# Kernel tuning notes

Measured on AMD Instinct MI355X. Metric: run time of the kernel, lower is better.

## Reference

```python
import jax, jax.numpy as jnp
import numpy as np

N_VERTS = 100000
N_JOINTS = 24
N_BETAS = 10
N_POSEDIRS = 207  # (24-1)*9
# Standard SMPL kinematic tree parents
PARENTS = np.array([-1, 0, 0, 0, 1, 2, 3, 4, 5, 6, 7, 8, 9, 9, 9, 12, 13, 14, 16, 17, 18, 19, 20, 21])


def setup_inputs() -> dict:
    key = jax.random.key(0)
    ks = jax.random.split(key, 9)
    f = jnp.float32
    return {
        "betas": jax.random.normal(ks[0], (N_BETAS,), f),
        "pose": jax.random.normal(ks[1], (N_JOINTS, 3), f) * 0.2,
        "scale": jnp.ones((1,), f),
        "trans": jax.random.normal(ks[2], (3,), f),
        "v_template": jax.random.normal(ks[3], (N_VERTS, 3), f),
        "shapedirs": jax.random.normal(ks[4], (N_VERTS, 3, N_BETAS), f) * 0.01,
        "posedirs": jax.random.normal(ks[5], (N_VERTS, 3, N_POSEDIRS), f) * 0.01,
        "J_regressor": jax.random.uniform(ks[6], (N_JOINTS, N_VERTS), f) / N_VERTS,
        "weights": jax.nn.softmax(jax.random.normal(ks[7], (N_VERTS, N_JOINTS), f), axis=-1),
    }


def rodrigues(r):
    """Axis-angle [J,3] -> rotation matrices [J,3,3] (matches torch impl; eps kept tiny+deterministic)."""
    theta = jnp.linalg.norm(r + 1e-8, axis=-1, keepdims=True)  # [J,1]
    r_hat = r / theta
    z = jnp.zeros_like(r_hat[:, 0])
    K = jnp.stack([z, -r_hat[:, 2], r_hat[:, 1],
                   r_hat[:, 2], z, -r_hat[:, 0],
                   -r_hat[:, 1], r_hat[:, 0], z], axis=1).reshape(-1, 3, 3)
    c = jnp.cos(theta)[..., None]  # [J,1,1]
    s = jnp.sin(theta)[..., None]
    outer = r_hat[:, :, None] * r_hat[:, None, :]  # [J,3,3]
    I = jnp.eye(3, dtype=r.dtype)
    return c * I + (1.0 - c) * outer + s * K


def reference(betas, pose, scale, trans, v_template, shapedirs, posedirs, J_regressor, weights):
    dt = v_template.dtype
    # blend shapes
    v_shaped = jnp.einsum('vks,s->vk', shapedirs, betas) + v_template  # [V,3]
    J = J_regressor @ v_shaped  # [24,3]
    R = rodrigues(pose)  # [24,3,3]
    I3 = jnp.eye(3, dtype=dt)
    lrotmin = (R[1:] - I3).reshape(-1)  # [207]
    v_posed = v_shaped + jnp.einsum('vkp,p->vk', posedirs, lrotmin)  # [V,3]
    # forward kinematics over 24-joint chain
    bottom = jnp.array([[0.0, 0.0, 0.0, 1.0]], dtype=dt)
    def make_A(Ri, t):
        return jnp.concatenate([jnp.concatenate([Ri, t[:, None]], axis=1), bottom], axis=0)  # [4,4]
    As = [make_A(R[0], J[0])]
    for i in range(1, N_JOINTS):
        p = int(PARENTS[i])
        As.append(As[p] @ make_A(R[i], J[i] - J[p]))
    G = jnp.stack(As)  # [24,4,4]
    # remove rest-pose joint locations
    Jh = jnp.concatenate([J, jnp.zeros((N_JOINTS, 1), dt)], axis=1)  # [24,4]
    corr = jnp.einsum('jab,jb->ja', G, Jh)  # [24,4]
    rel = G - jnp.concatenate([jnp.zeros((N_JOINTS, 4, 3), dt), corr[:, :, None]], axis=2)
    # linear blend skinning
    T = jnp.einsum('vj,jab->vab', weights, rel)  # [V,4,4]
    vh = jnp.concatenate([v_posed, jnp.ones((v_posed.shape[0], 1), dt)], axis=1)  # [V,4]
    v = jnp.einsum('vab,vb->va', T, vh)[:, :3]  # [V,3]
    return v * scale.reshape(()) + trans[None, :]
```

## Files before the change

kernel.cpp:

```cpp
#include <hip/hip_runtime.h>

#define NV 100000
#define NJ 24
#define NP 207
#define NPART 25
#define NQUADS (NV / 4)
#define GRIDF 512
#define NWV (GRIDF * 4)

__device__ __forceinline__ float dpp_red32(float x) {
  x += __int_as_float(__builtin_amdgcn_update_dpp(0, __float_as_int(x), 0x111, 0xf, 0xf, true));
  x += __int_as_float(__builtin_amdgcn_update_dpp(0, __float_as_int(x), 0x112, 0xf, 0xf, true));
  x += __int_as_float(__builtin_amdgcn_update_dpp(0, __float_as_int(x), 0x114, 0xf, 0xf, true));
  x += __int_as_float(__builtin_amdgcn_update_dpp(0, __float_as_int(x), 0x118, 0xf, 0xf, true));
  x += __int_as_float(__builtin_amdgcn_update_dpp(0, __float_as_int(x), 0x142, 0xf, 0xf, true));
  return x;
}

__global__ __launch_bounds__(256) void k_shape(
    const float* __restrict__ betas, const float* __restrict__ v_template,
    const float* __restrict__ shapedirs, float* __restrict__ v_shaped) {
  __shared__ float sb[10];
  if (threadIdx.x < 10) sb[threadIdx.x] = betas[threadIdx.x];
  __syncthreads();
  int t = blockIdx.x * 256 + threadIdx.x;
  if (t >= 3 * NV / 2) return;
  const float4* sd4 = (const float4*)(shapedirs + (size_t)t * 20);
  float4 f0 = sd4[0], f1 = sd4[1], f2 = sd4[2], f3 = sd4[3], f4v = sd4[4];
  float2 vt = ((const float2*)v_template)[t];
  float a = vt.x
          + f0.x * sb[0] + f0.y * sb[1] + f0.z * sb[2] + f0.w * sb[3]
          + f1.x * sb[4] + f1.y * sb[5] + f1.z * sb[6] + f1.w * sb[7]
          + f2.x * sb[8] + f2.y * sb[9];
  float b = vt.y
          + f2.z * sb[0] + f2.w * sb[1]
          + f3.x * sb[2] + f3.y * sb[3] + f3.z * sb[4] + f3.w * sb[5]
          + f4v.x * sb[6] + f4v.y * sb[7] + f4v.z * sb[8] + f4v.w * sb[9];
  ((float2*)v_shaped)[t] = make_float2(a, b);
}

__global__ __launch_bounds__(256) void k_jreg(
    const float* __restrict__ Jreg, const float* __restrict__ v_shaped,
    float* __restrict__ jpT) {
  int j = blockIdx.x, part = blockIdx.y, tid = threadIdx.x;
  const int SL = NV / NPART;
  int v0 = part * SL;
  const float4* w4 = (const float4*)(Jreg + (size_t)j * NV + v0);
  const float4* s4 = (const float4*)(v_shaped + (size_t)3 * v0);
  float s0 = 0.f, s1 = 0.f, s2 = 0.f;
  for (int i4 = tid; i4 < SL / 4; i4 += 256) {
    float4 w = w4[i4];
    float4 A = s4[3 * i4 + 0];
    float4 B = s4[3 * i4 + 1];
    float4 C = s4[3 * i4 + 2];
    s0 += w.x * A.x + w.y * A.w + w.z * B.z + w.w * C.y;
    s1 += w.x * A.y + w.y * B.x + w.z * B.w + w.w * C.z;
    s2 += w.x * A.z + w.y * B.y + w.z * C.x + w.w * C.w;
  }
  __shared__ float red[256][3];
  red[tid][0] = s0; red[tid][1] = s1; red[tid][2] = s2;
  __syncthreads();
  for (int off = 128; off > 0; off >>= 1) {
    if (tid < off) {
      red[tid][0] += red[tid + off][0];
      red[tid][1] += red[tid + off][1];
      red[tid][2] += red[tid + off][2];
    }
    __syncthreads();
  }
  if (tid < 3) jpT[(j * 3 + tid) * 32 + part] = red[0][tid];
}

__device__ __forceinline__ void stage_quad(float4* dst, const float4* src, int lane) {
  #pragma unroll
  for (int r = 0; r < 10; ++r) {
    int i4 = r * 64 + lane;
    int i4c = (i4 < 621) ? i4 : 620;
    __builtin_amdgcn_global_load_lds(
        (const __attribute__((address_space(1))) void*)(src + i4c),
        (__attribute__((address_space(3))) void*)(dst + r * 64),
        16, 0, 0);
  }
}

__global__ __launch_bounds__(256, 2) void k_fused(
    const float* __restrict__ posedirs, const float* __restrict__ wgt,
    const float* __restrict__ pose, const float* __restrict__ jpT,
    const float* __restrict__ scale, const float* __restrict__ trans,
    float* __restrict__ vbuf) {
  __shared__ float4 buf[4][2][640];
  int tid = threadIdx.x, b = blockIdx.x;
  int wid = tid >> 6, lane = tid & 63, half = lane >> 5, lj = lane & 31;
  int W = b * 4 + wid;
  const float4* pd4 = (const float4*)posedirs;

  int q0 = W;
  float pvl0 = (lj < 3) ? vbuf[(size_t)3 * (q0 * 4 + half) + lj] : 0.f;
  float wj0  = (lj < NJ) ? wgt[(size_t)(q0 * 4 + half) * NJ + lj] : 0.f;
  float pvl1 = (lj < 3) ? vbuf[(size_t)3 * (q0 * 4 + 2 + half) + lj] : 0.f;
  float wj1  = (lj < NJ) ? wgt[(size_t)(q0 * 4 + 2 + half) * NJ + lj] : 0.f;
  __builtin_amdgcn_sched_barrier(0);
  stage_quad(&buf[wid][0][0], pd4 + (size_t)q0 * 621, lane);

  float* fkJ  = (float*)&buf[0][1][0];
  float* fkR  = fkJ + 72;
  float* fkG  = fkJ + 288;
  float* lrs  = fkJ + 576;
  float* relS = fkJ + 784;
  if (tid < NJ * 3) {
    const float* src = jpT + tid * 32;
    float a = 0.f;
    #pragma unroll
    for (int i = 0; i < NPART; ++i) a += src[i];
    fkJ[tid] = a;
  }
  if (tid < NJ) {
    float rx = pose[tid * 3 + 0], ry = pose[tid * 3 + 1], rz = pose[tid * 3 + 2];
    float tx = rx + 1e-8f, ty = ry + 1e-8f, tz = rz + 1e-8f;
    float theta = sqrtf(tx * tx + ty * ty + tz * tz);
    float x = rx / theta, y = ry / theta, z = rz / theta;
    float c = cosf(theta), s = sinf(theta), C = 1.f - c;
    float Rr[9];
    Rr[0] = c + C * x * x;     Rr[1] = C * x * y - s * z; Rr[2] = C * x * z + s * y;
    Rr[3] = C * x * y + s * z; Rr[4] = c + C * y * y;     Rr[5] = C * y * z - s * x;
    Rr[6] = C * x * z - s * y; Rr[7] = C * y * z + s * x; Rr[8] = c + C * z * z;
    #pragma unroll
    for (int e = 0; e < 9; ++e) fkR[tid * 9 + e] = Rr[e];
    if (tid >= 1) {
      #pragma unroll
      for (int e = 0; e < 9; ++e) {
        float id = (e == 0 || e == 4 || e == 8) ? 1.f : 0.f;
        lrs[(tid - 1) * 9 + e] = Rr[e] - id;
      }
    }
  }
  __syncthreads();
  if (tid < 3) {
    const int par[NJ] = {-1,0,0,0,1,2,3,4,5,6,7,8,9,9,9,12,13,14,16,17,18,19,20,21};
    int a = tid;
    fkG[a * 4 + 0] = fkR[a * 3 + 0];
    fkG[a * 4 + 1] = fkR[a * 3 + 1];
    fkG[a * 4 + 2] = fkR[a * 3 + 2];
    fkG[a * 4 + 3] = fkJ[a];
    #pragma unroll
    for (int i = 1; i < NJ; ++i) {
      int p = par[i];
      float t0 = fkJ[i * 3 + 0] - fkJ[p * 3 + 0];
      float t1 = fkJ[i * 3 + 1] - fkJ[p * 3 + 1];
      float t2 = fkJ[i * 3 + 2] - fkJ[p * 3 + 2];
      float g0 = fkG[p * 12 + a * 4 + 0], g1 = fkG[p * 12 + a * 4 + 1];
      float g2 = fkG[p * 12 + a * 4 + 2], g3 = fkG[p * 12 + a * 4 + 3];
      fkG[i * 12 + a * 4 + 0] = g0 * fkR[i * 9 + 0] + g1 * fkR[i * 9 + 3] + g2 * fkR[i * 9 + 6];
      fkG[i * 12 + a * 4 + 1] = g0 * fkR[i * 9 + 1] + g1 * fkR[i * 9 + 4] + g2 * fkR[i * 9 + 7];
      fkG[i * 12 + a * 4 + 2] = g0 * fkR[i * 9 + 2] + g1 * fkR[i * 9 + 5] + g2 * fkR[i * 9 + 8];
      fkG[i * 12 + a * 4 + 3] = g3 + g0 * t0 + g1 * t1 + g2 * t2;
    }
  }
  __syncthreads();
  if (tid < NJ) {
    #pragma unroll
    for (int a = 0; a < 3; ++a) {
      float corr = fkG[tid * 12 + a * 4 + 0] * fkJ[tid * 3 + 0] +
                   fkG[tid * 12 + a * 4 + 1] * fkJ[tid * 3 + 1] +
                   fkG[tid * 12 + a * 4 + 2] * fkJ[tid * 3 + 2];
      relS[tid * 12 + a * 4 + 0] = fkG[tid * 12 + a * 4 + 0];
      relS[tid * 12 + a * 4 + 1] = fkG[tid * 12 + a * 4 + 1];
      relS[tid * 12 + a * 4 + 2] = fkG[tid * 12 + a * 4 + 2];
      relS[tid * 12 + a * 4 + 3] = fkG[tid * 12 + a * 4 + 3] - corr;
    }
  }
  __syncthreads();

  float llr[7];
  #pragma unroll
  for (int e = 0; e < 7; ++e) {
    int p = lj + 32 * e;
    llr[e] = (p < NP) ? lrs[p] : 0.f;
  }
  float rlq[12];
  #pragma unroll
  for (int e = 0; e < 12; ++e) rlq[e] = (lj < NJ) ? relS[lj * 12 + e] : 0.f;
  float sc = scale[0];
  float tr = (lj < 3) ? trans[lj] : 0.f;

  __syncthreads();
  asm volatile("s_waitcnt vmcnt(0)" ::: "memory");

  int nt = (NQUADS - 1 - W) / NWV + 1;
  for (int it = 0; it < nt; ++it) {
    int cur = it & 1;
    int qn = W + (it + 1) * NWV;
    if (qn >= NQUADS) qn = NQUADS - 1;
    float pvl0_n = (lj < 3) ? vbuf[(size_t)3 * (qn * 4 + half) + lj] : 0.f;
    float wj0_n  = (lj < NJ) ? wgt[(size_t)(qn * 4 + half) * NJ + lj] : 0.f;
    float pvl1_n = (lj < 3) ? vbuf[(size_t)3 * (qn * 4 + 2 + half) + lj] : 0.f;
    float wj1_n  = (lj < NJ) ? wgt[(size_t)(qn * 4 + 2 + half) * NJ + lj] : 0.f;
    __builtin_amdgcn_sched_barrier(0);
    stage_quad(&buf[wid][cur ^ 1][0], pd4 + (size_t)qn * 621, lane);
    asm volatile("s_waitcnt vmcnt(14)" ::: "memory");
    __builtin_amdgcn_sched_barrier(0);

    int q = W + it * NWV;
    const float* chunk = (const float*)&buf[wid][cur][0];
    #pragma unroll
    for (int h = 0; h < 2; ++h) {
      int vv = q * 4 + 2 * h + half;
      const float* row = chunk + (2 * h + half) * (3 * NP);
      float pvl = h ? pvl1 : pvl0;
      float wj  = h ? wj1 : wj0;
      float a0 = 0.f, a1 = 0.f, a2 = 0.f;
      #pragma unroll
      for (int e = 0; e < 7; ++e) {
        int p = lj + 32 * e;
        if (p < NP) {
          float l = llr[e];
          a0 += row[p] * l;
          a1 += row[NP + p] * l;
          a2 += row[2 * NP + p] * l;
        }
      }
      int gb = lane & 32;
      a0 = __shfl(dpp_red32(a0), gb + 31);
      a1 = __shfl(dpp_red32(a1), gb + 31);
      a2 = __shfl(dpp_red32(a2), gb + 31);
      float p0 = __shfl(pvl, gb + 0) + a0;
      float p1 = __shfl(pvl, gb + 1) + a1;
      float p2 = __shfl(pvl, gb + 2) + a2;
      float q0v = rlq[0] * p0 + rlq[1] * p1 + rlq[2]  * p2 + rlq[3];
      float q1v = rlq[4] * p0 + rlq[5] * p1 + rlq[6]  * p2 + rlq[7];
      float q2v = rlq[8] * p0 + rlq[9] * p1 + rlq[10] * p2 + rlq[11];
      float r0 = dpp_red32(wj * q0v);
      float r1 = dpp_red32(wj * q1v);
      float r2 = dpp_red32(wj * q2v);
      r0 = __shfl(r0, gb + 31);
      r1 = __shfl(r1, gb + 31);
      r2 = __shfl(r2, gb + 31);
      if (lj < 3) {
        float oo = (lj == 0) ? r0 : (lj == 1) ? r1 : r2;
        vbuf[(size_t)3 * vv + lj] = oo * sc + tr;
      }
    }
    pvl0 = pvl0_n; wj0 = wj0_n; pvl1 = pvl1_n; wj1 = wj1_n;
  }
  asm volatile("s_waitcnt vmcnt(0)" ::: "memory");
}

extern "C" void kernel_launch(void* const* d_in, const int* in_sizes, int n_in,
                              void* d_out, int out_size, void* d_ws, size_t ws_size,
                              hipStream_t stream) {
  const float* betas      = (const float*)d_in[0];
  const float* pose       = (const float*)d_in[1];
  const float* scale      = (const float*)d_in[2];
  const float* trans      = (const float*)d_in[3];
  const float* v_template = (const float*)d_in[4];
  const float* shapedirs  = (const float*)d_in[5];
  const float* posedirs   = (const float*)d_in[6];
  const float* Jreg       = (const float*)d_in[7];
  const float* weights    = (const float*)d_in[8];
  float* out = (float*)d_out;
  float* ws  = (float*)d_ws;

  float* jpT = ws;

  k_shape<<<(3 * NV / 2 + 255) / 256, 256, 0, stream>>>(betas, v_template, shapedirs, out);
  k_jreg<<<dim3(NJ, NPART), 256, 0, stream>>>(Jreg, out, jpT);
  k_fused<<<GRIDF, 256, 0, stream>>>(posedirs, weights, pose, jpT, scale, trans, out);
}
```

Before: 59.79 us.

## Process vertex pairs per wave with smaller LDS stages and higher occupancy

Each wave now stages two vertices of posedirs (1242 floats) per iteration instead of four, halving the LDS double buffer and doubling the grid. Odd pairs start at a non-16-byte-aligned offset, so the source is shifted back two floats and the row pointer offset compensates. Launch bounds go from 2 to 4 blocks per CU to raise occupancy for this memory-bound stream. The trade-off is more loop iterations, each with less work to hide latency, and slightly more over-fetch per vertex from the alignment padding.

```diff
diff --git a/kernel.cpp b/kernel.cpp
--- a/kernel.cpp
+++ b/kernel.cpp
@@ -4,8 +4,8 @@
 #define NJ 24
 #define NP 207
 #define NPART 25
-#define NQUADS (NV / 4)
-#define GRIDF 512
+#define NPAIRS (NV / 2)
+#define GRIDF 1024
 #define NWV (GRIDF * 4)
 
 __device__ __forceinline__ float dpp_red32(float x) {
@@ -71,11 +71,11 @@
   if (tid < 3) jpT[(j * 3 + tid) * 32 + part] = red[0][tid];
 }
 
-__device__ __forceinline__ void stage_quad(float4* dst, const float4* src, int lane) {
+__device__ __forceinline__ void stage_pair(float4* dst, const float4* src, int lane) {
   #pragma unroll
-  for (int r = 0; r < 10; ++r) {
+  for (int r = 0; r < 5; ++r) {
     int i4 = r * 64 + lane;
-    int i4c = (i4 < 621) ? i4 : 620;
+    int i4c = (i4 < 311) ? i4 : 310;
     __builtin_amdgcn_global_load_lds(
         (const __attribute__((address_space(1))) void*)(src + i4c),
         (__attribute__((address_space(3))) void*)(dst + r * 64),
@@ -83,24 +83,26 @@
   }
 }
 
-__global__ __launch_bounds__(256, 2) void k_fused(
+__device__ __forceinline__ const float4* pair_src(const float* posedirs, int p) {
+  size_t startf = (size_t)1242 * p - ((p & 1) ? 2 : 0);
+  return (const float4*)(posedirs + startf);
+}
+
+__global__ __launch_bounds__(256, 4) void k_fused(
     const float* __restrict__ posedirs, const float* __restrict__ wgt,
     const float* __restrict__ pose, const float* __restrict__ jpT,
     const float* __restrict__ scale, const float* __restrict__ trans,
     float* __restrict__ vbuf) {
-  __shared__ float4 buf[4][2][640];
+  __shared__ float4 buf[4][2][320];
   int tid = threadIdx.x, b = blockIdx.x;
   int wid = tid >> 6, lane = tid & 63, half = lane >> 5, lj = lane & 31;
   int W = b * 4 + wid;
-  const float4* pd4 = (const float4*)posedirs;
-
-  int q0 = W;
-  float pvl0 = (lj < 3) ? vbuf[(size_t)3 * (q0 * 4 + half) + lj] : 0.f;
-  float wj0  = (lj < NJ) ? wgt[(size_t)(q0 * 4 + half) * NJ + lj] : 0.f;
-  float pvl1 = (lj < 3) ? vbuf[(size_t)3 * (q0 * 4 + 2 + half) + lj] : 0.f;
-  float wj1  = (lj < NJ) ? wgt[(size_t)(q0 * 4 + 2 + half) * NJ + lj] : 0.f;
+  int sh = (W & 1) ? 2 : 0;
+
+  float pvl = (lj < 3) ? vbuf[(size_t)3 * (W * 2 + half) + lj] : 0.f;
+  float wj  = (lj < NJ) ? wgt[(size_t)(W * 2 + half) * NJ + lj] : 0.f;
   __builtin_amdgcn_sched_barrier(0);
-  stage_quad(&buf[wid][0][0], pd4 + (size_t)q0 * 621, lane);
+  stage_pair(&buf[wid][0][0], pair_src(posedirs, W), lane);
 
   float* fkJ  = (float*)&buf[0][1][0];
   float* fkR  = fkJ + 72;
@@ -186,61 +188,50 @@
   __syncthreads();
   asm volatile("s_waitcnt vmcnt(0)" ::: "memory");
 
-  int nt = (NQUADS - 1 - W) / NWV + 1;
+  int nt = (NPAIRS - 1 - W) / NWV + 1;
   for (int it = 0; it < nt; ++it) {
     int cur = it & 1;
-    int qn = W + (it + 1) * NWV;
-    if (qn >= NQUADS) qn = NQUADS - 1;
-    float pvl0_n = (lj < 3) ? vbuf[(size_t)3 * (qn * 4 + half) + lj] : 0.f;
-    float wj0_n  = (lj < NJ) ? wgt[(size_t)(qn * 4 + half) * NJ + lj] : 0.f;
-    float pvl1_n = (lj < 3) ? vbuf[(size_t)3 * (qn * 4 + 2 + half) + lj] : 0.f;
-    float wj1_n  = (lj < NJ) ? wgt[(size_t)(qn * 4 + 2 + half) * NJ + lj] : 0.f;
+    int pn = W + (it + 1) * NWV;
+    if (pn >= NPAIRS) pn = NPAIRS - 1;
+    float pvl_n = (lj < 3) ? vbuf[(size_t)3 * (pn * 2 + half) + lj] : 0.f;
+    float wj_n  = (lj < NJ) ? wgt[(size_t)(pn * 2 + half) * NJ + lj] : 0.f;
     __builtin_amdgcn_sched_barrier(0);
-    stage_quad(&buf[wid][cur ^ 1][0], pd4 + (size_t)qn * 621, lane);
-    asm volatile("s_waitcnt vmcnt(14)" ::: "memory");
+    stage_pair(&buf[wid][cur ^ 1][0], pair_src(posedirs, pn), lane);
+    asm volatile("s_waitcnt vmcnt(7)" ::: "memory");
     __builtin_amdgcn_sched_barrier(0);
 
-    int q = W + it * NWV;
-    const float* chunk = (const float*)&buf[wid][cur][0];
-    #pragma unroll
-    for (int h = 0; h < 2; ++h) {
-      int vv = q * 4 + 2 * h + half;
-      const float* row = chunk + (2 * h + half) * (3 * NP);
-      float pvl = h ? pvl1 : pvl0;
-      float wj  = h ? wj1 : wj0;
-      float a0 = 0.f, a1 = 0.f, a2 = 0.f;
-      #pragma unroll
-      for (int e = 0; e < 7; ++e) {
-        int p = lj + 32 * e;
-        if (p < NP) {
-          float l = llr[e];
-          a0 += row[p] * l;
-          a1 += row[NP + p] * l;
-          a2 += row[2 * NP + p] * l;
-        }
+    int p = W + it * NWV;
+    int vv = p * 2 + half;
+    const float* row = (const float*)&buf[wid][cur][0] + sh + half * (3 * NP);
+    float a0 = 0.f, a1 = 0.f, a2 = 0.f;
+    #pragma unroll
+    for (int e = 0; e < 7; ++e) {
+      int pp = lj + 32 * e;
+      if (pp < NP) {
+        float l = llr[e];
+        a0 += row[pp] * l;
+        a1 += row[NP + pp] * l;
+        a2 += row[2 * NP + pp] * l;
       }
-      int gb = lane & 32;
-      a0 = __shfl(dpp_red32(a0), gb + 31);
-      a1 = __shfl(dpp_red32(a1), gb + 31);
-      a2 = __shfl(dpp_red32(a2), gb + 31);
-      float p0 = __shfl(pvl, gb + 0) + a0;
-      float p1 = __shfl(pvl, gb + 1) + a1;
-      float p2 = __shfl(pvl, gb + 2) + a2;
-      float q0v = rlq[0] * p0 + rlq[1] * p1 + rlq[2]  * p2 + rlq[3];
-      float q1v = rlq[4] * p0 + rlq[5] * p1 + rlq[6]  * p2 + rlq[7];
-      float q2v = rlq[8] * p0 + rlq[9] * p1 + rlq[10] * p2 + rlq[11];
-      float r0 = dpp_red32(wj * q0v);
-      float r1 = dpp_red32(wj * q1v);
-      float r2 = dpp_red32(wj * q2v);
-      r0 = __shfl(r0, gb + 31);
-      r1 = __shfl(r1, gb + 31);
-      r2 = __shfl(r2, gb + 31);
-      if (lj < 3) {
-        float oo = (lj == 0) ? r0 : (lj == 1) ? r1 : r2;
-        vbuf[(size_t)3 * vv + lj] = oo * sc + tr;
-      }
-    }
-    pvl0 = pvl0_n; wj0 = wj0_n; pvl1 = pvl1_n; wj1 = wj1_n;
+    }
+    int gb = lane & 32;
+    a0 = __shfl(dpp_red32(a0), gb + 31);
+    a1 = __shfl(dpp_red32(a1), gb + 31);
+    a2 = __shfl(dpp_red32(a2), gb + 31);
+    float p0 = __shfl(pvl, gb + 0) + a0;
+    float p1 = __shfl(pvl, gb + 1) + a1;
+    float p2 = __shfl(pvl, gb + 2) + a2;
+    float q0v = rlq[0] * p0 + rlq[1] * p1 + rlq[2]  * p2 + rlq[3];
+    float q1v = rlq[4] * p0 + rlq[5] * p1 + rlq[6]  * p2 + rlq[7];
+    float q2v = rlq[8] * p0 + rlq[9] * p1 + rlq[10] * p2 + rlq[11];
+    float r0 = __shfl(dpp_red32(wj * q0v), gb + 31);
+    float r1 = __shfl(dpp_red32(wj * q1v), gb + 31);
+    float r2 = __shfl(dpp_red32(wj * q2v), gb + 31);
+    if (lj < 3) {
+      float oo = (lj == 0) ? r0 : (lj == 1) ? r1 : r2;
+      vbuf[(size_t)3 * vv + lj] = oo * sc + tr;
+    }
+    pvl = pvl_n; wj = wj_n;
   }
   asm volatile("s_waitcnt vmcnt(0)" ::: "memory");
 }
```

Result: faster. 58.36 us, median of 2 (-2.4%).
